# Performance work log

Hardware: AMD Instinct MI355X
Metric: run time of the kernel (lower is better)

## Reference

```python
import jax, jax.numpy as jnp
import numpy as np

TAU = 0.25    # membrane decay constant
VTH = 0.3     # firing threshold
ALPHA = 0.5   # surrogate-gradient window half-width


def spike(v):
    # Heaviside spike activation (forward only)
    return (v > 0).astype(v.dtype)


def setup_inputs() -> dict:
    key = jax.random.key(0)
    # [B, C, H, W, T] with time on the last dim, as the module expects
    x = jax.random.normal(key, (32, 128, 32, 32, 8), dtype=jnp.float32)
    return {"x": x}


def reference(x) -> jnp.ndarray:
    # LIF recurrence over the last (time) dimension:
    #   u_t = TAU * u_{t-1} * (1 - o_{t-1}) + x_t
    #   o_t = 1[u_t - VTH > 0]
    # Note: at step 0 the original reads out[..., 0] which is still zeros,
    # so o_prev = 0 initially.
    xT = jnp.moveaxis(x, -1, 0)                 # [T, B, C, H, W]
    u0 = jnp.zeros(x.shape[:-1], dtype=x.dtype)
    o0 = jnp.zeros(x.shape[:-1], dtype=x.dtype)

    def step(carry, x_t):
        u, o_prev = carry
        u = TAU * u * (1.0 - o_prev) + x_t
        o = spike(u - VTH)
        return (u, o), o

    _, outT = jax.lax.scan(step, (u0, o0), xT)  # [T, B, C, H, W]
    return jnp.moveaxis(outT, 0, -1)            # [B, C, H, W, T]
```

## Files before the change

kernel.cpp:

```cpp
#include <hip/hip_runtime.h>


#define LIF_TAU 0.25f
#define LIF_VTH 0.3f

__global__ __launch_bounds__(256) void lif_spike_kernel(
    const float* __restrict__ x, float* __restrict__ out, int n_neurons) {
    int tid = blockIdx.x * blockDim.x + threadIdx.x;
    if (tid >= n_neurons) return;

    const float4* xv = reinterpret_cast<const float4*>(x) + (size_t)tid * 2;
    float4 a = xv[0];
    float4 b = xv[1];
    float xs[8] = {a.x, a.y, a.z, a.w, b.x, b.y, b.z, b.w};

    float u = 0.0f;
    float o = 0.0f;
    float os[8];
#pragma unroll
    for (int t = 0; t < 8; ++t) {
        u = LIF_TAU * u * (1.0f - o) + xs[t];
        o = (u > LIF_VTH) ? 1.0f : 0.0f;
        os[t] = o;
    }

    float4* ov = reinterpret_cast<float4*>(out) + (size_t)tid * 2;
    ov[0] = make_float4(os[0], os[1], os[2], os[3]);
    ov[1] = make_float4(os[4], os[5], os[6], os[7]);
}

extern "C" void kernel_launch(void* const* d_in, const int* in_sizes, int n_in,
                              void* d_out, int out_size, void* d_ws, size_t ws_size,
                              hipStream_t stream) {
    const float* x = (const float*)d_in[0];
    float* out = (float*)d_out;
    int n_elems = in_sizes[0];
    int n_neurons = n_elems / 8;

    int block = 256;
    int grid = (n_neurons + block - 1) / block;
    lif_spike_kernel<<<grid, block, 0, stream>>>(x, out, n_neurons);
}
```

Measured before the change: 227.2 us.

## Stage LIF tiles through LDS for fully coalesced loads and nontemporal stores

Each block now loads its 256 neurons x 8 timesteps as contiguous float4 vectors, so consecutive threads read consecutive 16-byte chunks instead of 32-byte strides. The data is transposed through padded shared memory, the recurrence runs per neuron, and the result is transposed back before the store. Loads and stores use nontemporal builtins to bypass cache retention. This adds two barriers and LDS traffic, and it drops the bounds check, so the element count must be a multiple of 2048.

```diff
diff --git a/kernel.cpp b/kernel.cpp
--- a/kernel.cpp
+++ b/kernel.cpp
@@ -3,30 +3,57 @@
 
 #define LIF_TAU 0.25f
 #define LIF_VTH 0.3f
+#define T_STEPS 8
+#define BLOCK 256
+#define ROW 257
 
-__global__ __launch_bounds__(256) void lif_spike_kernel(
-    const float* __restrict__ x, float* __restrict__ out, int n_neurons) {
-    int tid = blockIdx.x * blockDim.x + threadIdx.x;
-    if (tid >= n_neurons) return;
+typedef float v4f __attribute__((ext_vector_type(4)));
 
-    const float4* xv = reinterpret_cast<const float4*>(x) + (size_t)tid * 2;
-    float4 a = xv[0];
-    float4 b = xv[1];
-    float xs[8] = {a.x, a.y, a.z, a.w, b.x, b.y, b.z, b.w};
+__global__ __launch_bounds__(BLOCK) void lif_spike_kernel(
+    const float* __restrict__ x, float* __restrict__ out) {
+    __shared__ float lds[T_STEPS * ROW];
 
-    float u = 0.0f;
-    float o = 0.0f;
-    float os[8];
+    const int t = threadIdx.x;
+    const size_t blk4 = (size_t)blockIdx.x * (BLOCK * T_STEPS / 4);
+    const v4f* __restrict__ xv = reinterpret_cast<const v4f*>(x) + blk4;
+    v4f* __restrict__ ov = reinterpret_cast<v4f*>(out) + blk4;
+
+    v4f v0 = __builtin_nontemporal_load(xv + t);
+    v4f v1 = __builtin_nontemporal_load(xv + t + BLOCK);
+
+    const int n0 = t >> 1;
+    const int tb = (t & 1) * 4;
+    lds[(tb + 0) * ROW + n0] = v0.x;
+    lds[(tb + 1) * ROW + n0] = v0.y;
+    lds[(tb + 2) * ROW + n0] = v0.z;
+    lds[(tb + 3) * ROW + n0] = v0.w;
+    lds[(tb + 0) * ROW + n0 + 128] = v1.x;
+    lds[(tb + 1) * ROW + n0 + 128] = v1.y;
+    lds[(tb + 2) * ROW + n0 + 128] = v1.z;
+    lds[(tb + 3) * ROW + n0 + 128] = v1.w;
+    __syncthreads();
+
+    float u = 0.0f, o = 0.0f;
 #pragma unroll
-    for (int t = 0; t < 8; ++t) {
-        u = LIF_TAU * u * (1.0f - o) + xs[t];
+    for (int k = 0; k < T_STEPS; ++k) {
+        float xk = lds[k * ROW + t];
+        u = LIF_TAU * u * (1.0f - o) + xk;
         o = (u > LIF_VTH) ? 1.0f : 0.0f;
-        os[t] = o;
+        lds[k * ROW + t] = o;
     }
+    __syncthreads();
 
-    float4* ov = reinterpret_cast<float4*>(out) + (size_t)tid * 2;
-    ov[0] = make_float4(os[0], os[1], os[2], os[3]);
-    ov[1] = make_float4(os[4], os[5], os[6], os[7]);
+    v4f w0, w1;
+    w0.x = lds[(tb + 0) * ROW + n0];
+    w0.y = lds[(tb + 1) * ROW + n0];
+    w0.z = lds[(tb + 2) * ROW + n0];
+    w0.w = lds[(tb + 3) * ROW + n0];
+    w1.x = lds[(tb + 0) * ROW + n0 + 128];
+    w1.y = lds[(tb + 1) * ROW + n0 + 128];
+    w1.z = lds[(tb + 2) * ROW + n0 + 128];
+    w1.w = lds[(tb + 3) * ROW + n0 + 128];
+    __builtin_nontemporal_store(w0, ov + t);
+    __builtin_nontemporal_store(w1, ov + t + BLOCK);
 }
 
 extern "C" void kernel_launch(void* const* d_in, const int* in_sizes, int n_in,
@@ -35,9 +62,7 @@
     const float* x = (const float*)d_in[0];
     float* out = (float*)d_out;
     int n_elems = in_sizes[0];
-    int n_neurons = n_elems / 8;
+    int n_blocks = n_elems / (BLOCK * T_STEPS);
 
-    int block = 256;
-    int grid = (n_neurons + block - 1) / block;
-    lif_spike_kernel<<<grid, block, 0, stream>>>(x, out, n_neurons);
+    lif_spike_kernel<<<n_blocks, BLOCK, 0, stream>>>(x, out);
 }
```

Result: faster. 217.3 us (-4.3%).

## Split each neuron across two lanes with shuffle handoff and nontemporal vec4 I/O

Applied to the files above, without the earlier changes.

Each thread now loads one float4 (half a neuron's 8 time steps) instead of two, so adjacent lanes share a neuron. Even lanes run steps 0-3 and hand their final membrane and spike state to the odd lane via __shfl_xor. Each lane then re-runs its 4 steps, the odd lane starting from the received state. Loads and stores use nontemporal builtins, giving fully coalesced 16-byte accesses per lane. The bounds check is removed and the grid is computed by floor division, which assumes the element count is a multiple of 1024.

```diff
diff --git a/kernel.cpp b/kernel.cpp
--- a/kernel.cpp
+++ b/kernel.cpp
@@ -3,30 +3,41 @@
 
 #define LIF_TAU 0.25f
 #define LIF_VTH 0.3f
+#define BLOCK 256
 
-__global__ __launch_bounds__(256) void lif_spike_kernel(
-    const float* __restrict__ x, float* __restrict__ out, int n_neurons) {
-    int tid = blockIdx.x * blockDim.x + threadIdx.x;
-    if (tid >= n_neurons) return;
+typedef float v4f __attribute__((ext_vector_type(4)));
 
-    const float4* xv = reinterpret_cast<const float4*>(x) + (size_t)tid * 2;
-    float4 a = xv[0];
-    float4 b = xv[1];
-    float xs[8] = {a.x, a.y, a.z, a.w, b.x, b.y, b.z, b.w};
+__global__ __launch_bounds__(BLOCK) void lif_spike_kernel(
+    const float* __restrict__ x, float* __restrict__ out) {
+    const size_t g = (size_t)blockIdx.x * BLOCK + threadIdx.x;
 
-    float u = 0.0f;
-    float o = 0.0f;
-    float os[8];
+    const v4f* __restrict__ xv = reinterpret_cast<const v4f*>(x);
+    v4f* __restrict__ ov = reinterpret_cast<v4f*>(out);
+
+    v4f v = __builtin_nontemporal_load(xv + g);
+
+    float u = 0.0f, o = 0.0f;
 #pragma unroll
-    for (int t = 0; t < 8; ++t) {
-        u = LIF_TAU * u * (1.0f - o) + xs[t];
+    for (int k = 0; k < 4; ++k) {
+        u = LIF_TAU * u * (1.0f - o) + v[k];
         o = (u > LIF_VTH) ? 1.0f : 0.0f;
-        os[t] = o;
     }
 
-    float4* ov = reinterpret_cast<float4*>(out) + (size_t)tid * 2;
-    ov[0] = make_float4(os[0], os[1], os[2], os[3]);
-    ov[1] = make_float4(os[4], os[5], os[6], os[7]);
+    float cu = __shfl_xor(u, 1);
+    float co = __shfl_xor(o, 1);
+    const bool odd = (threadIdx.x & 1) != 0;
+    u = odd ? cu : 0.0f;
+    o = odd ? co : 0.0f;
+
+    v4f w;
+#pragma unroll
+    for (int k = 0; k < 4; ++k) {
+        u = LIF_TAU * u * (1.0f - o) + v[k];
+        o = (u > LIF_VTH) ? 1.0f : 0.0f;
+        w[k] = o;
+    }
+
+    __builtin_nontemporal_store(w, ov + g);
 }
 
 extern "C" void kernel_launch(void* const* d_in, const int* in_sizes, int n_in,
@@ -35,9 +46,8 @@
     const float* x = (const float*)d_in[0];
     float* out = (float*)d_out;
     int n_elems = in_sizes[0];
-    int n_neurons = n_elems / 8;
+    int n_vec4 = n_elems / 4;
+    int n_blocks = n_vec4 / BLOCK;
 
-    int block = 256;
-    int grid = (n_neurons + block - 1) / block;
-    lif_spike_kernel<<<grid, block, 0, stream>>>(x, out, n_neurons);
+    lif_spike_kernel<<<n_blocks, BLOCK, 0, stream>>>(x, out);
 }
```

New measurement: 216.0 us. 4.9% less time.
